# Kernel optimization log

Hardware: AMD Instinct MI355X
Metric: run time of the kernel (lower is better)

Reference implementation:

```python
import jax, jax.numpy as jnp
import numpy as np

D_MODEL = 1024
N_HEADS = 16
D_K = D_MODEL // N_HEADS


def setup_inputs() -> dict:
    key = jax.random.key(0)
    ks = jax.random.split(key, 9)
    s = 0.02
    x = jax.random.normal(ks[0], (2, 2048, D_MODEL), dtype=jnp.float32)
    Wq = jax.random.normal(ks[1], (D_MODEL, D_MODEL), dtype=jnp.float32) * s
    bq = jax.random.normal(ks[2], (D_MODEL,), dtype=jnp.float32) * s
    Wk = jax.random.normal(ks[3], (D_MODEL, D_MODEL), dtype=jnp.float32) * s
    bk = jax.random.normal(ks[4], (D_MODEL,), dtype=jnp.float32) * s
    Wv = jax.random.normal(ks[5], (D_MODEL, D_MODEL), dtype=jnp.float32) * s
    bv = jax.random.normal(ks[6], (D_MODEL,), dtype=jnp.float32) * s
    Wo = jax.random.normal(ks[7], (D_MODEL, D_MODEL), dtype=jnp.float32) * s
    bo = jax.random.normal(ks[8], (D_MODEL,), dtype=jnp.float32) * s
    return {"x": x, "Wq": Wq, "bq": bq, "Wk": Wk, "bk": bk,
            "Wv": Wv, "bv": bv, "Wo": Wo, "bo": bo}


def reference(x, Wq, bq, Wk, bk, Wv, bv, Wo, bo):
    B, S, D = x.shape
    # nn.Linear: y = x @ W.T + b
    q = x @ Wq.T + bq  # [B,S,D]
    k = x @ Wk.T + bk
    v = x @ Wv.T + bv
    # split heads -> [B,H,S,dk]
    q = q.reshape(B, S, N_HEADS, D_K).transpose(0, 2, 1, 3)
    k = k.reshape(B, S, N_HEADS, D_K).transpose(0, 2, 1, 3)
    v = v.reshape(B, S, N_HEADS, D_K).transpose(0, 2, 1, 3)
    scale = 1.0 / jnp.sqrt(jnp.asarray(D_K, dtype=x.dtype))
    scores = jnp.einsum('bhqd,bhkd->bhqk', q, k) * scale  # [B,H,S,S]
    weights = jax.nn.softmax(scores, axis=-1)
    out = jnp.einsum('bhqk,bhkd->bhqd', weights, v)  # [B,H,S,dk]
    concat = out.transpose(0, 2, 1, 3).reshape(B, S, D)
    return concat @ Wo.T + bo
```

## Files before the change

### kernel.cpp

```cpp
#include <hip/hip_runtime.h>

typedef unsigned short ushort_t;
typedef __attribute__((ext_vector_type(8))) __bf16 bf16x8;
typedef __attribute__((ext_vector_type(4))) float floatx4;

#define AS1 __attribute__((address_space(1)))
#define AS3 __attribute__((address_space(3)))

#define D_MODEL 1024
#define NH 16
#define DKH 64
#define SEQ 2048
#define NB 2
#define MTOT (NB * SEQ)

#define QSCALE 0.18033688011112042f

#define OFF_X   0u
#define OFF_WQ  4194304u
#define OFF_BQ  5242880u
#define OFF_WK  5243904u
#define OFF_BK  6292480u
#define OFF_WV  6293504u
#define OFF_BV  7342080u
#define OFF_WO  7343104u
#define OFF_BO  8391680u
#define CVT_TOT 8392704u

__device__ __forceinline__ float bf2f(ushort_t u) {
    union { unsigned u; float f; } v; v.u = ((unsigned)u) << 16; return v.f;
}
__device__ __forceinline__ ushort_t f2bf(float f) {
    union { float f; unsigned u; } v; v.f = f;
    unsigned r = v.u + 0x7FFFu + ((v.u >> 16) & 1u);
    return (ushort_t)(r >> 16);
}
__device__ __forceinline__ unsigned pack2bf(float a, float b) {
    unsigned ua = __float_as_uint(a), ub = __float_as_uint(b);
    ua = ua + 0x7FFFu + ((ua >> 16) & 1u);
    ub = ub + 0x7FFFu + ((ub >> 16) & 1u);
    return __builtin_amdgcn_perm(ub, ua, 0x07060302);
}
__device__ __forceinline__ float fexp2(float x) { return __builtin_amdgcn_exp2f(x); }

__global__ __launch_bounds__(256) void convert_kernel(
    const float* __restrict__ x,  const float* __restrict__ wq, const float* __restrict__ bq_,
    const float* __restrict__ wk, const float* __restrict__ bk_, const float* __restrict__ wv,
    const float* __restrict__ bv_, const float* __restrict__ wo, const float* __restrict__ bo_,
    ushort_t* __restrict__ dst)
{
    const unsigned idx = ((unsigned)blockIdx.x * 256u + threadIdx.x) * 4u;
    if (idx >= CVT_TOT) return;
    const float* src; unsigned off;
    if      (idx < OFF_WQ) { src = x;   off = idx - OFF_X;  }
    else if (idx < OFF_BQ) { src = wq;  off = idx - OFF_WQ; }
    else if (idx < OFF_WK) { src = bq_; off = idx - OFF_BQ; }
    else if (idx < OFF_BK) { src = wk;  off = idx - OFF_WK; }
    else if (idx < OFF_WV) { src = bk_; off = idx - OFF_BK; }
    else if (idx < OFF_BV) { src = wv;  off = idx - OFF_WV; }
    else if (idx < OFF_WO) { src = bv_; off = idx - OFF_BV; }
    else if (idx < OFF_BO) { src = wo;  off = idx - OFF_WO; }
    else                   { src = bo_; off = idx - OFF_BO; }
    float4 v = *reinterpret_cast<const float4*>(src + off);
    uint2 p;
    p.x = pack2bf(v.x, v.y);
    p.y = pack2bf(v.z, v.w);
    *reinterpret_cast<uint2*>(dst + idx) = p;
}

__device__ __forceinline__ void gemm_core(
    const ushort_t* __restrict__ X, const ushort_t* __restrict__ W,
    int m0, int n0, ushort_t* lds, floatx4 acc[4][4])
{
    const int tid = threadIdx.x;
    const int lane = tid & 63, wv = tid >> 6;
    const int wm = (wv >> 1) * 64, wn = (wv & 1) * 64;
    const int l15 = lane & 15, quad = lane >> 4;
    const floatx4 z4 = {0.f, 0.f, 0.f, 0.f};
#pragma unroll
    for (int i = 0; i < 4; ++i)
#pragma unroll
        for (int j = 0; j < 4; ++j) acc[i][j] = z4;
    const int lrow = lane >> 2;
    const int lcol = (lane & 3) * 8;
    const ushort_t* gA = X + (size_t)(m0 + lrow) * D_MODEL + lcol;
    const ushort_t* gB = W + (size_t)(n0 + lrow) * D_MODEL + lcol;

#pragma unroll
    for (int j = 0; j < 2; ++j) {
        const int r0 = (wv * 2 + j) * 16;
        __builtin_amdgcn_global_load_lds(
            (const AS1 unsigned*)(gA + (size_t)r0 * D_MODEL),
            (AS3 unsigned*)(lds + r0 * 32), 16, 0, 0);
        __builtin_amdgcn_global_load_lds(
            (const AS1 unsigned*)(gB + (size_t)r0 * D_MODEL),
            (AS3 unsigned*)(lds + 4096 + r0 * 32), 16, 0, 0);
    }
    asm volatile("s_waitcnt vmcnt(0)" ::: "memory");
    __syncthreads();

#pragma unroll 2
    for (int t = 0; t < 32; ++t) {
        const int cur = t & 1;
        ushort_t* L = lds + cur * 8192;
        if (t < 31) {
            ushort_t* Ln = lds + (cur ^ 1) * 8192;
            const int k0 = (t + 1) * 32;
#pragma unroll
            for (int j = 0; j < 2; ++j) {
                const int r0 = (wv * 2 + j) * 16;
                __builtin_amdgcn_global_load_lds(
                    (const AS1 unsigned*)(gA + (size_t)r0 * D_MODEL + k0),
                    (AS3 unsigned*)(Ln + r0 * 32), 16, 0, 0);
                __builtin_amdgcn_global_load_lds(
                    (const AS1 unsigned*)(gB + (size_t)r0 * D_MODEL + k0),
                    (AS3 unsigned*)(Ln + 4096 + r0 * 32), 16, 0, 0);
            }
        }
        bf16x8 af[4], bfr[4];
#pragma unroll
        for (int i = 0; i < 4; ++i)
            af[i] = *reinterpret_cast<const bf16x8*>(L + (wm + i * 16 + l15) * 32 + quad * 8);
#pragma unroll
        for (int j = 0; j < 4; ++j)
            bfr[j] = *reinterpret_cast<const bf16x8*>(L + 4096 + (wn + j * 16 + l15) * 32 + quad * 8);
#pragma unroll
        for (int i = 0; i < 4; ++i)
#pragma unroll
            for (int j = 0; j < 4; ++j)
                acc[i][j] = __builtin_amdgcn_mfma_f32_16x16x32_bf16(af[i], bfr[j], acc[i][j], 0, 0, 0);
        asm volatile("s_waitcnt vmcnt(0)" ::: "memory");
        __syncthreads();
    }
}

__global__ __launch_bounds__(256, 3) void qkv_kernel(
    const ushort_t* __restrict__ x,
    const ushort_t* __restrict__ Wq, const ushort_t* __restrict__ bq,
    const ushort_t* __restrict__ Wk, const ushort_t* __restrict__ bk,
    const ushort_t* __restrict__ Wv, const ushort_t* __restrict__ bv,
    ushort_t* __restrict__ q_ws, ushort_t* __restrict__ k_ws, ushort_t* __restrict__ vt_ws)
{
    __shared__ __align__(16) ushort_t lds[17408];
    const int m0 = blockIdx.x * 128;
    const int which = blockIdx.y >> 3;
    const int n0 = (blockIdx.y & 7) * 128;
    const ushort_t* W    = (which == 0) ? Wq : (which == 1) ? Wk : Wv;
    const ushort_t* bias = (which == 0) ? bq : (which == 1) ? bk : bv;
    floatx4 acc[4][4];
    gemm_core(x, W, m0, n0, lds, acc);
    const int tid = threadIdx.x, lane = tid & 63, wv = tid >> 6;
    const int wm = (wv >> 1) * 64, wn = (wv & 1) * 64;
    const int l15 = lane & 15, quad = lane >> 4;
    const int b0 = m0 >> 11;
    const int s0 = m0 & (SEQ - 1);
    __syncthreads();
    if (which < 2) {
        ushort_t* Ts = lds;
        ushort_t* dst = (which == 0) ? q_ws : k_ws;
        const float scl = (which == 0) ? QSCALE : 1.0f;
#pragma unroll
        for (int j = 0; j < 4; ++j) {
            int coln = wn + j * 16 + l15;
            float bb = bf2f(bias[n0 + coln]);
#pragma unroll
            for (int i = 0; i < 4; ++i)
#pragma unroll
                for (int r = 0; r < 4; ++r) {
                    int rowm = wm + i * 16 + quad * 4 + r;
                    Ts[rowm * 136 + coln] = f2bf((acc[i][j][r] + bb) * scl);
                }
        }
        __syncthreads();
#pragma unroll
        for (int i = 0; i < 8; ++i) {
            int c = tid + 256 * i;
            int rowm = c >> 4, chunk = c & 15;
            float4 v = *reinterpret_cast<const float4*>(Ts + rowm * 136 + chunk * 8);
            int s = s0 + rowm;
            int n = n0 + chunk * 8, h = n >> 6, d = n & 63;
            *reinterpret_cast<float4*>(dst + (((size_t)(b0 * NH + h)) * SEQ + s) * DKH + d) = v;
        }
    } else {
        ushort_t* Ts = lds;
#pragma unroll
        for (int j = 0; j < 4; ++j) {
            int coln = wn + j * 16 + l15;
            float bb = bf2f(bias[n0 + coln]);
#pragma unroll
            for (int i = 0; i < 4; ++i)
#pragma unroll
                for (int r = 0; r < 4; ++r) {
                    int rowm = wm + i * 16 + quad * 4 + r;
                    Ts[coln * 136 + rowm] = f2bf(acc[i][j][r] + bb);
                }
        }
        __syncthreads();
#pragma unroll
        for (int i = 0; i < 8; ++i) {
            int c = tid + 256 * i;
            int nr = c >> 4, mc = (c & 15) * 8;
            float4 v = *reinterpret_cast<const float4*>(Ts + nr * 136 + mc);
            int n = n0 + nr, h = n >> 6, d = n & 63;
            *reinterpret_cast<float4*>(vt_ws + (((size_t)(b0 * NH + h)) * DKH + d) * SEQ + s0 + mc) = v;
        }
    }
}

__global__ __launch_bounds__(512, 4) void attn_kernel(
    const ushort_t* __restrict__ q_ws, const ushort_t* __restrict__ k_ws,
    const ushort_t* __restrict__ vt_ws, ushort_t* __restrict__ concat)
{
    __shared__ __align__(16) ushort_t sm[36864];
    const int qb = blockIdx.x, bh = blockIdx.y;
    const int tid = threadIdx.x;
    const int lane = tid & 63, wv = tid >> 6;
    const int half = wv >> 2, wq = wv & 3;
    const int l15 = lane & 15, quad = lane >> 4;
    const int ht = tid & 255;

    const ushort_t* Qg = q_ws + ((size_t)bh * SEQ + qb * 128) * DKH;
    const ushort_t* Kg = k_ws + ((size_t)bh * SEQ + half * (SEQ / 2)) * DKH;
    const ushort_t* Vg = vt_ws + (size_t)bh * DKH * SEQ + half * (SEQ / 2);

    ushort_t* Ks     = sm + half * 4608;
    ushort_t* VTs    = sm + 9216 + half * 4608;
    ushort_t* Ps     = sm + 18432 + wv * 2304;
    ushort_t* Qstage = sm + 18432;

    const int r0c = ht >> 3,         c0c = (ht & 7) * 8;
    const int r1c = (ht + 256) >> 3, c1c = ((ht + 256) & 7) * 8;

#pragma unroll
    for (int i = 0; i < 2; ++i) {
        int c = tid + 512 * i;
        int row = c >> 3, col = (c & 7) * 8;
        *reinterpret_cast<float4*>(Qstage + row * 72 + col) =
            *reinterpret_cast<const float4*>(Qg + row * DKH + col);
    }
    __syncthreads();
    bf16x8 aq[2][2];
#pragma unroll
    for (int nt = 0; nt < 2; ++nt)
#pragma unroll
        for (int ks = 0; ks < 2; ++ks)
            aq[nt][ks] = *reinterpret_cast<const bf16x8*>(Qstage + (wq * 32 + nt * 16 + l15) * 72 + ks * 32 + quad * 8);

    const floatx4 z4 = {0.f, 0.f, 0.f, 0.f};
    floatx4 o[2][4];
    floatx4 la4[2] = {z4, z4};
#pragma unroll
    for (int nt = 0; nt < 2; ++nt)
#pragma unroll
        for (int dt = 0; dt < 4; ++dt) o[nt][dt] = z4;

    float4 pk0 = *reinterpret_cast<const float4*>(Kg + (size_t)r0c * DKH + c0c);
    float4 pk1 = *reinterpret_cast<const float4*>(Kg + (size_t)r1c * DKH + c1c);
    float4 pv0 = *reinterpret_cast<const float4*>(Vg + (size_t)r0c * SEQ + c0c);
    float4 pv1 = *reinterpret_cast<const float4*>(Vg + (size_t)r1c * SEQ + c1c);

    for (int t = 0; t < 16; ++t) {
        __syncthreads();
        *reinterpret_cast<float4*>(Ks + r0c * 72 + c0c) = pk0;
        *reinterpret_cast<float4*>(Ks + r1c * 72 + c1c) = pk1;
        *reinterpret_cast<float4*>(VTs + r0c * 72 + c0c) = pv0;
        *reinterpret_cast<float4*>(VTs + r1c * 72 + c1c) = pv1;
        __syncthreads();
        if (t < 15) {
            int toff = (t + 1) * 64;
            pk0 = *reinterpret_cast<const float4*>(Kg + (size_t)(toff + r0c) * DKH + c0c);
            pk1 = *reinterpret_cast<const float4*>(Kg + (size_t)(toff + r1c) * DKH + c1c);
            pv0 = *reinterpret_cast<const float4*>(Vg + (size_t)r0c * SEQ + toff + c0c);
            pv1 = *reinterpret_cast<const float4*>(Vg + (size_t)r1c * SEQ + toff + c1c);
        }

        floatx4 st[2][4];
#pragma unroll
        for (int mt = 0; mt < 4; ++mt) {
            bf16x8 akf = *reinterpret_cast<const bf16x8*>(Ks + (mt * 16 + l15) * 72 + quad * 8);
            st[0][mt] = __builtin_amdgcn_mfma_f32_16x16x32_bf16(akf, aq[0][0], z4, 0, 0, 0);
            st[1][mt] = __builtin_amdgcn_mfma_f32_16x16x32_bf16(akf, aq[1][0], z4, 0, 0, 0);
        }
#pragma unroll
        for (int mt = 0; mt < 4; ++mt) {
            bf16x8 akf = *reinterpret_cast<const bf16x8*>(Ks + (mt * 16 + l15) * 72 + 32 + quad * 8);
            st[0][mt] = __builtin_amdgcn_mfma_f32_16x16x32_bf16(akf, aq[0][1], st[0][mt], 0, 0, 0);
            st[1][mt] = __builtin_amdgcn_mfma_f32_16x16x32_bf16(akf, aq[1][1], st[1][mt], 0, 0, 0);
        }

#pragma unroll
        for (int nt = 0; nt < 2; ++nt)
#pragma unroll
            for (int mt = 0; mt < 4; ++mt) {
#pragma unroll
                for (int r = 0; r < 4; ++r) st[nt][mt][r] = fexp2(st[nt][mt][r]);
                la4[nt] += st[nt][mt];
                uint2 pk;
                pk.x = pack2bf(st[nt][mt][0], st[nt][mt][1]);
                pk.y = pack2bf(st[nt][mt][2], st[nt][mt][3]);
                *reinterpret_cast<uint2*>(Ps + (nt * 16 + l15) * 72 + mt * 16 + quad * 4) = pk;
            }
        asm volatile("s_waitcnt lgkmcnt(0)" ::: "memory");
#pragma unroll
        for (int ks = 0; ks < 2; ++ks) {
            bf16x8 ap0 = *reinterpret_cast<const bf16x8*>(Ps + l15 * 72 + ks * 32 + quad * 8);
            bf16x8 ap1 = *reinterpret_cast<const bf16x8*>(Ps + (16 + l15) * 72 + ks * 32 + quad * 8);
#pragma unroll
            for (int dt = 0; dt < 4; ++dt) {
                bf16x8 bvv = *reinterpret_cast<const bf16x8*>(VTs + (dt * 16 + l15) * 72 + ks * 32 + quad * 8);
                o[0][dt] = __builtin_amdgcn_mfma_f32_16x16x32_bf16(ap0, bvv, o[0][dt], 0, 0, 0);
                o[1][dt] = __builtin_amdgcn_mfma_f32_16x16x32_bf16(ap1, bvv, o[1][dt], 0, 0, 0);
            }
        }
    }
    float lsum[2];
#pragma unroll
    for (int nt = 0; nt < 2; ++nt) {
        float s = la4[nt][0] + la4[nt][1] + la4[nt][2] + la4[nt][3];
        s += __shfl_xor(s, 16, 64);
        s += __shfl_xor(s, 32, 64);
        lsum[nt] = s;
    }
    __syncthreads();
    float* Of = (float*)sm;
    float* lf = Of + 128 * 68;
    if (half == 1) {
#pragma unroll
        for (int nt = 0; nt < 2; ++nt) {
            if (quad == 0) lf[wq * 32 + nt * 16 + l15] = lsum[nt];
#pragma unroll
            for (int r = 0; r < 4; ++r) {
                int row = wq * 32 + nt * 16 + quad * 4 + r;
#pragma unroll
                for (int dt = 0; dt < 4; ++dt)
                    Of[row * 68 + dt * 16 + l15] = o[nt][dt][r];
            }
        }
    }
    __syncthreads();
    if (half == 0) {
        const int b0 = bh >> 4, h = bh & 15;
#pragma unroll
        for (int nt = 0; nt < 2; ++nt) {
            float ltot = lsum[nt] + lf[wq * 32 + nt * 16 + l15];
            float linv = 1.f / ltot;
#pragma unroll
            for (int r = 0; r < 4; ++r) {
                float lB = __shfl(linv, quad * 4 + r, 64);
                int row = wq * 32 + nt * 16 + quad * 4 + r;
                size_t base = ((size_t)(b0 * SEQ + qb * 128 + row)) * D_MODEL + h * DKH;
#pragma unroll
                for (int dt = 0; dt < 4; ++dt) {
                    float sum = o[nt][dt][r] + Of[row * 68 + dt * 16 + l15];
                    concat[base + dt * 16 + l15] = f2bf(sum * lB);
                }
            }
        }
    }
}

__global__ __launch_bounds__(256, 3) void oproj_kernel(
    const ushort_t* __restrict__ cc, const ushort_t* __restrict__ Wo,
    const ushort_t* __restrict__ bo, float* __restrict__ out)
{
    __shared__ __align__(16) ushort_t lds[16384];
    const int m0 = blockIdx.x * 128, n0 = blockIdx.y * 128;
    floatx4 acc[4][4];
    gemm_core(cc, Wo, m0, n0, lds, acc);
    const int tid = threadIdx.x, lane = tid & 63, wv = tid >> 6;
    const int wm = (wv >> 1) * 64, wn = (wv & 1) * 64;
    const int l15 = lane & 15, quad = lane >> 4;
#pragma unroll
    for (int j = 0; j < 4; ++j) {
        int n = n0 + wn + j * 16 + l15;
        float bb = bf2f(bo[n]);
#pragma unroll
        for (int i = 0; i < 4; ++i)
#pragma unroll
            for (int r = 0; r < 4; ++r) {
                int m = m0 + wm + i * 16 + quad * 4 + r;
                out[(size_t)m * D_MODEL + n] = acc[i][j][r] + bb;
            }
    }
}

extern "C" void kernel_launch(void* const* d_in, const int* in_sizes, int n_in,
                              void* d_out, int out_size, void* d_ws, size_t ws_size,
                              hipStream_t stream)
{
    ushort_t* cvt = (ushort_t*)d_ws;
    const ushort_t* xb  = cvt + OFF_X;
    const ushort_t* Wqb = cvt + OFF_WQ;
    const ushort_t* bqb = cvt + OFF_BQ;
    const ushort_t* Wkb = cvt + OFF_WK;
    const ushort_t* bkb = cvt + OFF_BK;
    const ushort_t* Wvb = cvt + OFF_WV;
    const ushort_t* bvb = cvt + OFF_BV;
    const ushort_t* Wob = cvt + OFF_WO;
    const ushort_t* bob = cvt + OFF_BO;
    ushort_t* q_ws   = cvt + CVT_TOT;
    ushort_t* k_ws   = q_ws  + (size_t)MTOT * D_MODEL;
    ushort_t* vt_ws  = k_ws  + (size_t)MTOT * D_MODEL;
    ushort_t* concat = vt_ws + (size_t)MTOT * D_MODEL;

    convert_kernel<<<(CVT_TOT / 1024), 256, 0, stream>>>(
        (const float*)d_in[0], (const float*)d_in[1], (const float*)d_in[2],
        (const float*)d_in[3], (const float*)d_in[4], (const float*)d_in[5],
        (const float*)d_in[6], (const float*)d_in[7], (const float*)d_in[8], cvt);
    qkv_kernel<<<dim3(32, 24), 256, 0, stream>>>(xb, Wqb, bqb, Wkb, bkb, Wvb, bvb, q_ws, k_ws, vt_ws);
    attn_kernel<<<dim3(16, 32), 512, 0, stream>>>(q_ws, k_ws, vt_ws, concat);
    oproj_kernel<<<dim3(32, 8), 256, 0, stream>>>(concat, Wob, bob, (float*)d_out);
}
```

Measured before the change: 191.4 us.

## Triple-buffer GEMM k-loop and remap block indices for XCD-aware L2 locality

Replaces the double-buffered GEMM k-loop with a three-stage LDS ring. Each step waits only for the older stage's loads (vmcnt(4)) before issuing the next prefetch, so two tiles of global-to-LDS loads stay in flight during MFMA work. Also flattens the qkv, attention and output-projection grids to 1D and remaps block IDs so blocks that share operands are grouped, aiming to improve L2 reuse across the interleaved XCDs. LDS per block grows to 48KB for the GEMMs, which may cut occupancy, and the fixed vmcnt counts depend on the exact number of loads per stage.

```diff
diff --git a/kernel.cpp b/kernel.cpp
--- a/kernel.cpp
+++ b/kernel.cpp
@@ -42,6 +42,12 @@
     return __builtin_amdgcn_perm(ub, ua, 0x07060302);
 }
 __device__ __forceinline__ float fexp2(float x) { return __builtin_amdgcn_exp2f(x); }
+
+#define GSYNC(N) do { \
+    asm volatile("s_waitcnt vmcnt(" #N ")" ::: "memory"); \
+    __builtin_amdgcn_s_barrier(); \
+    __builtin_amdgcn_sched_barrier(0); \
+} while (0)
 
 __global__ __launch_bounds__(256) void convert_kernel(
     const float* __restrict__ x,  const float* __restrict__ wq, const float* __restrict__ bq_,
@@ -86,37 +92,19 @@
     const ushort_t* gA = X + (size_t)(m0 + lrow) * D_MODEL + lcol;
     const ushort_t* gB = W + (size_t)(n0 + lrow) * D_MODEL + lcol;
 
-#pragma unroll
-    for (int j = 0; j < 2; ++j) {
-        const int r0 = (wv * 2 + j) * 16;
-        __builtin_amdgcn_global_load_lds(
-            (const AS1 unsigned*)(gA + (size_t)r0 * D_MODEL),
-            (AS3 unsigned*)(lds + r0 * 32), 16, 0, 0);
-        __builtin_amdgcn_global_load_lds(
-            (const AS1 unsigned*)(gB + (size_t)r0 * D_MODEL),
-            (AS3 unsigned*)(lds + 4096 + r0 * 32), 16, 0, 0);
-    }
-    asm volatile("s_waitcnt vmcnt(0)" ::: "memory");
-    __syncthreads();
-
-#pragma unroll 2
-    for (int t = 0; t < 32; ++t) {
-        const int cur = t & 1;
-        ushort_t* L = lds + cur * 8192;
-        if (t < 31) {
-            ushort_t* Ln = lds + (cur ^ 1) * 8192;
-            const int k0 = (t + 1) * 32;
-#pragma unroll
-            for (int j = 0; j < 2; ++j) {
-                const int r0 = (wv * 2 + j) * 16;
-                __builtin_amdgcn_global_load_lds(
-                    (const AS1 unsigned*)(gA + (size_t)r0 * D_MODEL + k0),
-                    (AS3 unsigned*)(Ln + r0 * 32), 16, 0, 0);
-                __builtin_amdgcn_global_load_lds(
-                    (const AS1 unsigned*)(gB + (size_t)r0 * D_MODEL + k0),
-                    (AS3 unsigned*)(Ln + 4096 + r0 * 32), 16, 0, 0);
-            }
-        }
+    auto STAGE = [&](ushort_t* Ln, int k0) {
+#pragma unroll
+        for (int j = 0; j < 2; ++j) {
+            const int r0 = (wv * 2 + j) * 16;
+            __builtin_amdgcn_global_load_lds(
+                (const AS1 unsigned*)(gA + (size_t)r0 * D_MODEL + k0),
+                (AS3 unsigned*)(Ln + r0 * 32), 16, 0, 0);
+            __builtin_amdgcn_global_load_lds(
+                (const AS1 unsigned*)(gB + (size_t)r0 * D_MODEL + k0),
+                (AS3 unsigned*)(Ln + 4096 + r0 * 32), 16, 0, 0);
+        }
+    };
+    auto COMPUTE = [&](const ushort_t* L) {
         bf16x8 af[4], bfr[4];
 #pragma unroll
         for (int i = 0; i < 4; ++i)
@@ -129,9 +117,21 @@
 #pragma unroll
             for (int j = 0; j < 4; ++j)
                 acc[i][j] = __builtin_amdgcn_mfma_f32_16x16x32_bf16(af[i], bfr[j], acc[i][j], 0, 0, 0);
-        asm volatile("s_waitcnt vmcnt(0)" ::: "memory");
-        __syncthreads();
-    }
+    };
+
+    ushort_t* b0 = lds;
+    ushort_t* b1 = lds + 8192;
+    ushort_t* b2 = lds + 16384;
+
+    STAGE(b0, 0);
+    STAGE(b1, 32);
+    for (int tt = 0; tt < 30; tt += 3) {
+        GSYNC(4); STAGE(b2, (tt + 2) * 32); COMPUTE(b0);
+        GSYNC(4); STAGE(b0, (tt + 3) * 32); COMPUTE(b1);
+        GSYNC(4); STAGE(b1, (tt + 4) * 32); COMPUTE(b2);
+    }
+    GSYNC(4); COMPUTE(b0);
+    GSYNC(0); COMPUTE(b1);
 }
 
 __global__ __launch_bounds__(256, 3) void qkv_kernel(
@@ -141,10 +141,13 @@
     const ushort_t* __restrict__ Wv, const ushort_t* __restrict__ bv,
     ushort_t* __restrict__ q_ws, ushort_t* __restrict__ k_ws, ushort_t* __restrict__ vt_ws)
 {
-    __shared__ __align__(16) ushort_t lds[17408];
-    const int m0 = blockIdx.x * 128;
-    const int which = blockIdx.y >> 3;
-    const int n0 = (blockIdx.y & 7) * 128;
+    __shared__ __align__(16) ushort_t lds[24576];
+    const int L = blockIdx.x;
+    const int m_idx = (L & 7) + 8 * ((L >> 3) & 3);
+    const int y = L >> 5;
+    const int m0 = m_idx * 128;
+    const int which = y >> 3;
+    const int n0 = (y & 7) * 128;
     const ushort_t* W    = (which == 0) ? Wq : (which == 1) ? Wk : Wv;
     const ushort_t* bias = (which == 0) ? bq : (which == 1) ? bk : bv;
     floatx4 acc[4][4];
@@ -212,7 +215,9 @@
     const ushort_t* __restrict__ vt_ws, ushort_t* __restrict__ concat)
 {
     __shared__ __align__(16) ushort_t sm[36864];
-    const int qb = blockIdx.x, bh = blockIdx.y;
+    const int L = blockIdx.x;
+    const int qb = (L >> 3) & 15;
+    const int bh = (L & 7) + ((L >> 7) << 3);
     const int tid = threadIdx.x;
     const int lane = tid & 63, wv = tid >> 6;
     const int half = wv >> 2, wq = wv & 3;
@@ -363,8 +368,11 @@
     const ushort_t* __restrict__ cc, const ushort_t* __restrict__ Wo,
     const ushort_t* __restrict__ bo, float* __restrict__ out)
 {
-    __shared__ __align__(16) ushort_t lds[16384];
-    const int m0 = blockIdx.x * 128, n0 = blockIdx.y * 128;
+    __shared__ __align__(16) ushort_t lds[24576];
+    const int L = blockIdx.x;
+    const int m_idx = (L & 7) + 8 * (L >> 6);
+    const int n_idx = (L >> 3) & 7;
+    const int m0 = m_idx * 128, n0 = n_idx * 128;
     floatx4 acc[4][4];
     gemm_core(cc, Wo, m0, n0, lds, acc);
     const int tid = threadIdx.x, lane = tid & 63, wv = tid >> 6;
@@ -407,7 +415,7 @@
         (const float*)d_in[0], (const float*)d_in[1], (const float*)d_in[2],
         (const float*)d_in[3], (const float*)d_in[4], (const float*)d_in[5],
         (const float*)d_in[6], (const float*)d_in[7], (const float*)d_in[8], cvt);
-    qkv_kernel<<<dim3(32, 24), 256, 0, stream>>>(xb, Wqb, bqb, Wkb, bkb, Wvb, bvb, q_ws, k_ws, vt_ws);
-    attn_kernel<<<dim3(16, 32), 512, 0, stream>>>(q_ws, k_ws, vt_ws, concat);
-    oproj_kernel<<<dim3(32, 8), 256, 0, stream>>>(concat, Wob, bob, (float*)d_out);
-}
+    qkv_kernel<<<dim3(768), 256, 0, stream>>>(xb, Wqb, bqb, Wkb, bkb, Wvb, bvb, q_ws, k_ws, vt_ws);
+    attn_kernel<<<dim3(512), 512, 0, stream>>>(q_ws, k_ws, vt_ws, concat);
+    oproj_kernel<<<dim3(256), 256, 0, stream>>>(concat, Wob, bob, (float*)d_out);
+}
```

Result: no change. 190.2 us (-0.6%).
